# Performance work log

Hardware: AMD Instinct MI355X
Metric: run time of the kernel (lower is better)

## Reference

```python
import jax, jax.numpy as jnp
import numpy as np

B, T, D, H = 2, 2048, 2048, 16
HD = D // H


def setup_inputs() -> dict:
    key = jax.random.key(0)
    ks = jax.random.split(key, 6)
    s = 1.0 / np.sqrt(D)
    return {
        "x": jax.random.normal(ks[0], (B, T, D), dtype=jnp.float32),
        "Wq": jax.random.normal(ks[1], (D, D), dtype=jnp.float32) * s,
        "Wk": jax.random.normal(ks[2], (D, D), dtype=jnp.float32) * s,
        "Wv": jax.random.normal(ks[3], (D, D), dtype=jnp.float32) * s,
        "Wo": jax.random.normal(ks[4], (D, D), dtype=jnp.float32) * s,
        "bo": jnp.zeros((D,), dtype=jnp.float32),
    }


def reference(x, Wq, Wk, Wv, Wo, bo):
    b, t, d = x.shape
    # projections (torch Linear: x @ W.T)
    q = (x @ Wq.T).reshape(b, t, H, HD).transpose(0, 2, 1, 3)  # [B,H,T,HD]
    k = (x @ Wk.T).reshape(b, t, H, HD).transpose(0, 2, 1, 3)
    v = (x @ Wv.T).reshape(b, t, H, HD).transpose(0, 2, 1, 3)
    scores = jnp.einsum('bhid,bhjd->bhij', q, k) / np.sqrt(HD)  # [B,H,T,T]
    causal = jnp.tril(jnp.ones((t, t), dtype=bool))
    scores = jnp.where(causal[None, None], scores, -jnp.inf)
    attn = jax.nn.softmax(scores, axis=-1)
    out = jnp.einsum('bhij,bhjd->bhid', attn, v)  # [B,H,T,HD]
    out = out.transpose(0, 2, 1, 3).reshape(b, t, d)
    return out @ Wo.T + bo
```

## Files before the change

### kernel.cpp

```cpp
#include <hip/hip_runtime.h>
#include <hip/hip_bf16.h>

#define T_ 2048
#define D_ 2048
#define H_ 16
#define HD_ 128

typedef __hip_bfloat16 bf16;
using bf16x8 = __attribute__((ext_vector_type(8))) short;
using f32x4  = __attribute__((ext_vector_type(4))) float;

#define GLL16(g, l) __builtin_amdgcn_global_load_lds( \
    (const __attribute__((address_space(1))) void*)(g), \
    (__attribute__((address_space(3))) void*)(l), 16, 0, 0)

__device__ __forceinline__ f32x4 mfma16(bf16x8 a, bf16x8 b, f32x4 c) {
    return __builtin_amdgcn_mfma_f32_16x16x32_bf16(a, b, c, 0, 0, 0);
}

__global__ __launch_bounds__(256) void cast6(
    const float* __restrict__ s0, const float* __restrict__ s1,
    const float* __restrict__ s2, const float* __restrict__ s3,
    const float* __restrict__ s4, const float* __restrict__ s5,
    bf16* __restrict__ dst)
{
    int z = blockIdx.y;
    const float* s = (z == 0) ? s0 : (z == 1) ? s1 : (z == 2) ? s2
                   : (z == 3) ? s3 : (z == 4) ? s4 : s5;
    long i = ((long)blockIdx.x * 256 + threadIdx.x) * 8;
    float4 a = *(const float4*)(s + i);
    float4 b = *(const float4*)(s + i + 4);
    union { bf16 h[8]; int4 v; } u;
    u.h[0] = __float2bfloat16(a.x); u.h[1] = __float2bfloat16(a.y);
    u.h[2] = __float2bfloat16(a.z); u.h[3] = __float2bfloat16(a.w);
    u.h[4] = __float2bfloat16(b.x); u.h[5] = __float2bfloat16(b.y);
    u.h[6] = __float2bfloat16(b.z); u.h[7] = __float2bfloat16(b.w);
    *(int4*)(dst + (long)z * 4194304 + i) = u.v;
}


#define SA(t, h, b) do { \
    GLL16(Ab0 + (long)(h)*262144 + (t)*64,          &Asm[b][h][tid*8]); \
    GLL16(Ab0 + (long)(h)*262144 + 131072 + (t)*64, &Asm[b][h][4096 + tid*8]); \
} while (0)
#define SB(t, h, b) do { \
    GLL16(Bb0 + (long)(h)*262144 + (t)*64,          &Bsm[b][h][tid*8]); \
    GLL16(Bb0 + (long)(h)*262144 + 131072 + (t)*64, &Bsm[b][h][4096 + tid*8]); \
} while (0)

#define RA(mf, ks) (*(const bf16x8*)&Asm[buf][wr][((mf)*16 + l15)*64 + ((((ks)*32) + g8) ^ swF)])
#define RB(nf, ks) (*(const bf16x8*)&Bsm[buf][wc>>1][((wc&1)*64 + (nf)*16 + l15)*64 + ((((ks)*32) + g8) ^ swF)])

#define PH_SYNC() do { \
    __builtin_amdgcn_s_barrier(); \
    asm volatile("s_waitcnt lgkmcnt(0)" ::: "memory"); \
    __builtin_amdgcn_sched_barrier(0); \
} while (0)

__global__ __launch_bounds__(512) void gemm_qkv256(
    const bf16* __restrict__ xb, const bf16* __restrict__ Wall,
    bf16* __restrict__ QKV)
{
    __shared__ bf16 Asm[2][2][8192];
    __shared__ bf16 Bsm[2][2][8192];
    int tid = threadIdx.x, lane = tid & 63, wid = tid >> 6;
    int wr = wid >> 2, wc = wid & 3;
    int orig = blockIdx.x;
    int wg = (orig & 7) * 48 + (orig >> 3);
    int bm = wg / 24, bn = wg - bm * 24;

    int sr  = tid >> 3;
    int sc  = (((tid & 7) ^ (sr & 7)) * 8);
    const bf16* Ab0 = xb   + ((long)(bm * 256 + sr)) * 2048 + sc;
    const bf16* Bb0 = Wall + ((long)(bn * 256 + sr)) * 2048 + sc;

    int l15 = lane & 15, g8 = (lane >> 4) * 8;
    int swF = (l15 & 7) << 3;

    f32x4 acc[8][4];
    #pragma unroll
    for (int i = 0; i < 8; ++i)
        #pragma unroll
        for (int j = 0; j < 4; ++j) acc[i][j] = f32x4{0.f, 0.f, 0.f, 0.f};

    bf16x8 Ar[8][2];
    bf16x8 Br[4][2];

    SA(0, 0, 0); SA(0, 1, 0); SB(0, 0, 0); SB(0, 1, 0);
    SA(1, 0, 1); SA(1, 1, 1);
    asm volatile("s_waitcnt vmcnt(4)" ::: "memory");
    __builtin_amdgcn_s_barrier();

    const int NT = D_ / 64;
    for (int t = 0; t < NT; ++t) {
        int buf = t & 1, nbuf = buf ^ 1;
        #pragma unroll
        for (int mf = 0; mf < 4; ++mf) { Ar[mf][0] = RA(mf, 0); Ar[mf][1] = RA(mf, 1); }
        #pragma unroll
        for (int nf = 0; nf < 2; ++nf) { Br[nf][0] = RB(nf, 0); Br[nf][1] = RB(nf, 1); }
        if (t + 1 < NT) SB(t + 1, 0, nbuf);
        PH_SYNC();
        __builtin_amdgcn_s_setprio(1);
        #pragma unroll
        for (int mf = 0; mf < 4; ++mf)
            #pragma unroll
            for (int nf = 0; nf < 2; ++nf) {
                acc[mf][nf] = mfma16(Ar[mf][0], Br[nf][0], acc[mf][nf]);
                acc[mf][nf] = mfma16(Ar[mf][1], Br[nf][1], acc[mf][nf]);
            }
        __builtin_amdgcn_s_setprio(0);
        __builtin_amdgcn_s_barrier();
        #pragma unroll
        for (int mf = 4; mf < 8; ++mf) { Ar[mf][0] = RA(mf, 0); Ar[mf][1] = RA(mf, 1); }
        if (t + 1 < NT) SB(t + 1, 1, nbuf);
        PH_SYNC();
        __builtin_amdgcn_s_setprio(1);
        #pragma unroll
        for (int mf = 4; mf < 8; ++mf)
            #pragma unroll
            for (int nf = 0; nf < 2; ++nf) {
                acc[mf][nf] = mfma16(Ar[mf][0], Br[nf][0], acc[mf][nf]);
                acc[mf][nf] = mfma16(Ar[mf][1], Br[nf][1], acc[mf][nf]);
            }
        __builtin_amdgcn_s_setprio(0);
        __builtin_amdgcn_s_barrier();
        #pragma unroll
        for (int nf = 2; nf < 4; ++nf) { Br[nf][0] = RB(nf, 0); Br[nf][1] = RB(nf, 1); }
        if (t + 2 < NT) SA(t + 2, 0, buf);
        PH_SYNC();
        __builtin_amdgcn_s_setprio(1);
        #pragma unroll
        for (int mf = 0; mf < 4; ++mf)
            #pragma unroll
            for (int nf = 2; nf < 4; ++nf) {
                acc[mf][nf] = mfma16(Ar[mf][0], Br[nf][0], acc[mf][nf]);
                acc[mf][nf] = mfma16(Ar[mf][1], Br[nf][1], acc[mf][nf]);
            }
        __builtin_amdgcn_s_setprio(0);
        __builtin_amdgcn_s_barrier();
        if (t + 2 < NT) {
            SA(t + 2, 1, buf);
            asm volatile("s_waitcnt vmcnt(4)" ::: "memory");
        } else {
            asm volatile("s_waitcnt vmcnt(0)" ::: "memory");
        }
        __builtin_amdgcn_s_barrier();
        __builtin_amdgcn_s_setprio(1);
        #pragma unroll
        for (int mf = 4; mf < 8; ++mf)
            #pragma unroll
            for (int nf = 2; nf < 4; ++nf) {
                acc[mf][nf] = mfma16(Ar[mf][0], Br[nf][0], acc[mf][nf]);
                acc[mf][nf] = mfma16(Ar[mf][1], Br[nf][1], acc[mf][nf]);
            }
        __builtin_amdgcn_s_setprio(0);
        __builtin_amdgcn_s_barrier();
    }

    int mBase = bm * 256 + wr * 128;
    int nBase = bn * 256 + wc * 64;
    #pragma unroll
    for (int mf = 0; mf < 8; ++mf) {
        #pragma unroll
        for (int nf = 0; nf < 4; ++nf) {
            int n = nBase + nf * 16 + l15;
            int z = n >> 11, n2 = n & 2047;
            int h = n2 >> 7, hd = n2 & 127;
            #pragma unroll
            for (int r = 0; r < 4; ++r) {
                int m = mBase + mf * 16 + (lane >> 4) * 4 + r;
                int b = m >> 11, tt = m & 2047;
                QKV[(long)z * 8388608 + (((long)(b * H_ + h)) * T_ + tt) * HD_ + hd] =
                    __float2bfloat16(acc[mf][nf][r]);
            }
        }
    }
}


#define STAGE(t, b) do { \
    const bf16* Ag_ = Abase + (t)*32; \
    const bf16* Bg_ = Bbase + (t)*32; \
    GLL16(Ag_ + aoff0, As[b] + w*512); \
    GLL16(Ag_ + aoff1, As[b] + 2048 + w*512); \
    GLL16(Bg_ + aoff0, Bs[b] + w*512); \
    GLL16(Bg_ + aoff1, Bs[b] + 2048 + w*512); \
} while (0)

#define GEMM_MAINLOOP() \
    int tid = threadIdx.x, lane = tid & 63, w = tid >> 6; \
    int wm = w >> 1, wn = w & 1; \
    int srow = w*16 + (lane >> 2); \
    int scol = ((((lane & 3) - (srow >> 1)) & 3)) * 8; \
    long aoff0 = (long)srow * D_ + scol; \
    long aoff1 = aoff0 + 64L * D_; \
    f32x4 acc[4][4]; \
    _Pragma("unroll") \
    for (int i = 0; i < 4; ++i) \
        _Pragma("unroll") \
        for (int j = 0; j < 4; ++j) acc[i][j] = f32x4{0.f,0.f,0.f,0.f}; \
    STAGE(0, 0); STAGE(1, 1); STAGE(2, 2); \
    for (int kt = 0; kt < D_/32; ++kt) { \
        int rem = D_/32 - 1 - kt; \
        if (rem >= 2)      asm volatile("s_waitcnt vmcnt(8)" ::: "memory"); \
        else if (rem == 1) asm volatile("s_waitcnt vmcnt(4)" ::: "memory"); \
        else               asm volatile("s_waitcnt vmcnt(0)" ::: "memory"); \
        __builtin_amdgcn_s_barrier(); \
        asm volatile("" ::: "memory"); \
        int cb = kt & 3; \
        int g = lane >> 4; \
        bf16x8 af[4], bfr[4]; \
        _Pragma("unroll") \
        for (int mt = 0; mt < 4; ++mt) { \
            int r = wm*64 + mt*16 + (lane & 15); \
            af[mt] = *(const bf16x8*)&As[cb][r*32 + (((g + (r >> 1)) & 3) * 8)]; \
        } \
        _Pragma("unroll") \
        for (int nt = 0; nt < 4; ++nt) { \
            int r = wn*64 + nt*16 + (lane & 15); \
            bfr[nt] = *(const bf16x8*)&Bs[cb][r*32 + (((g + (r >> 1)) & 3) * 8)]; \
        } \
        if (kt + 3 < D_/32) { STAGE(kt + 3, (kt + 3) & 3); } \
        __builtin_amdgcn_s_setprio(1); \
        _Pragma("unroll") \
        for (int mt = 0; mt < 4; ++mt) \
            _Pragma("unroll") \
            for (int nt = 0; nt < 4; ++nt) \
                acc[mt][nt] = mfma16(af[mt], bfr[nt], acc[mt][nt]); \
        __builtin_amdgcn_s_setprio(0); \
    }

__global__ __launch_bounds__(256) void attn(
    const bf16* __restrict__ Qm, const bf16* __restrict__ Km, const bf16* __restrict__ Vm,
    bf16* __restrict__ Om)
{
    __shared__ bf16 Ks[64*136];
    __shared__ bf16 Vt[128*72];
    __shared__ bf16 Ps[128*72];
    int bm = 15 - (blockIdx.x >> 5);
    int bh = blockIdx.x & 31;
    int tid = threadIdx.x, lane = tid & 63, w = tid >> 6;
    const float c1 = 0.12754012780914427f;
    const float c2 = 23.083120654223414f;
    const bf16* Qb = Qm + (long)bh*T_*HD_;
    const bf16* Kb = Km + (long)bh*T_*HD_;
    const bf16* Vb = Vm + (long)bh*T_*HD_;
    int m0 = bm*128 + w*32;

    bf16x8 qf[2][4];
    #pragma unroll
    for (int mt = 0; mt < 2; ++mt)
        #pragma unroll
        for (int ks = 0; ks < 4; ++ks)
            qf[mt][ks] = *(const bf16x8*)(Qb + (long)(m0 + mt*16 + (lane & 15))*HD_ + ks*32 + (lane >> 4)*8);

    bf16x8 onesB;
    {
        short v1 = ((lane & 15) == 0) ? (short)0x3F80 : (short)0;
        #pragma unroll
        for (int jj = 0; jj < 8; ++jj) onesB[jj] = v1;
    }

    f32x4 oacc[2][8];
    f32x4 lacc[2];
    #pragma unroll
    for (int mt = 0; mt < 2; ++mt) {
        lacc[mt] = f32x4{0.f,0.f,0.f,0.f};
        #pragma unroll
        for (int dt = 0; dt < 8; ++dt) oacc[mt][dt] = f32x4{0.f,0.f,0.f,0.f};
    }

    int krow = (tid >> 4);
    int kcg  = tid & 15;
    int njt = 2*bm + 2;

    bf16x8 kreg[4], vreg[4];
    #pragma unroll
    for (int i = 0; i < 4; ++i) {
        kreg[i] = *(const bf16x8*)(Kb + (long)(i*16 + krow)*HD_ + kcg*8);
        vreg[i] = *(const bf16x8*)(Vb + (long)lane*HD_ + (w + i*4)*8);
    }

    for (int j = 0; j < njt; ++j) {
        int j0 = j*64;
        __syncthreads();
        #pragma unroll
        for (int i = 0; i < 4; ++i)
            *(bf16x8*)&Ks[(i*16 + krow)*136 + kcg*8] = kreg[i];
        #pragma unroll
        for (int i = 0; i < 4; ++i) {
            int dg = w + i*4;
            union { bf16 h[8]; bf16x8 v; } u;
            u.v = vreg[i];
            #pragma unroll
            for (int jj = 0; jj < 8; ++jj)
                Vt[(dg*8 + jj)*72 + lane] = u.h[jj];
        }
        __syncthreads();

        if (j + 1 < njt) {
            int jn0 = j0 + 64;
            #pragma unroll
            for (int i = 0; i < 4; ++i) {
                kreg[i] = *(const bf16x8*)(Kb + (long)(jn0 + i*16 + krow)*HD_ + kcg*8);
                vreg[i] = *(const bf16x8*)(Vb + (long)(jn0 + lane)*HD_ + (w + i*4)*8);
            }
        }

        bool anyv  = (j0 <= m0 + 31);
        if (anyv) {
            bool bmask = (j0 + 63 > m0);
            f32x4 s[2][4];
            #pragma unroll
            for (int mt = 0; mt < 2; ++mt)
                #pragma unroll
                for (int nt = 0; nt < 4; ++nt) s[mt][nt] = f32x4{0.f,0.f,0.f,0.f};
            #pragma unroll
            for (int ks = 0; ks < 4; ++ks) {
                bf16x8 kf[4];
                #pragma unroll
                for (int nt = 0; nt < 4; ++nt)
                    kf[nt] = *(const bf16x8*)&Ks[(nt*16 + (lane & 15))*136 + ks*32 + (lane >> 4)*8];
                #pragma unroll
                for (int mt = 0; mt < 2; ++mt)
                    #pragma unroll
                    for (int nt = 0; nt < 4; ++nt)
                        s[mt][nt] = mfma16(qf[mt][ks], kf[nt], s[mt][nt]);
            }
            #pragma unroll
            for (int mt = 0; mt < 2; ++mt) {
                #pragma unroll
                for (int nt = 0; nt < 4; ++nt) {
                    int n = j0 + nt*16 + (lane & 15);
                    #pragma unroll
                    for (int r = 0; r < 4; ++r) {
                        float x = s[mt][nt][r] * c1 - c2;
                        if (bmask) {
                            int mg = m0 + mt*16 + (lane >> 4)*4 + r;
                            x = (n <= mg) ? x : -1e30f;
                        }
                        float p = exp2f(x);
                        int prow = w*32 + mt*16 + (lane >> 4)*4 + r;
                        Ps[prow*72 + nt*16 + (lane & 15)] = __float2bfloat16(p);
                    }
                }
            }
            #pragma unroll
            for (int kn = 0; kn < 2; ++kn) {
                bf16x8 pf[2], vf[8];
                #pragma unroll
                for (int mt = 0; mt < 2; ++mt)
                    pf[mt] = *(const bf16x8*)&Ps[(w*32 + mt*16 + (lane & 15))*72 + kn*32 + (lane >> 4)*8];
                #pragma unroll
                for (int dt = 0; dt < 8; ++dt)
                    vf[dt] = *(const bf16x8*)&Vt[(dt*16 + (lane & 15))*72 + kn*32 + (lane >> 4)*8];
                #pragma unroll
                for (int mt = 0; mt < 2; ++mt)
                    lacc[mt] = mfma16(pf[mt], onesB, lacc[mt]);
                #pragma unroll
                for (int mt = 0; mt < 2; ++mt)
                    #pragma unroll
                    for (int dt = 0; dt < 8; ++dt)
                        oacc[mt][dt] = mfma16(pf[mt], vf[dt], oacc[mt][dt]);
            }
        }
    }
    int b = bh >> 4, h = bh & 15;
    #pragma unroll
    for (int mt = 0; mt < 2; ++mt) {
        #pragma unroll
        for (int r = 0; r < 4; ++r) {
            float l = __shfl(lacc[mt][r], lane & 48, 64);
            float inv = 1.f / l;
            int t = m0 + mt*16 + (lane >> 4)*4 + r;
            #pragma unroll
            for (int dt = 0; dt < 8; ++dt) {
                int d = dt*16 + (lane & 15);
                Om[((long)(b*T_ + t))*D_ + h*HD_ + d] = __float2bfloat16(oacc[mt][dt][r] * inv);
            }
        }
    }
}

__global__ __launch_bounds__(256) void gemm_out(
    const bf16* __restrict__ Ab, const bf16* __restrict__ Wob,
    const float* __restrict__ bo, float* __restrict__ out)
{
    __shared__ bf16 As[4][128*32];
    __shared__ bf16 Bs[4][128*32];
    int bn = blockIdx.x, bm = blockIdx.y;
    const bf16* Abase = Ab  + (long)bm * 128 * D_;
    const bf16* Bbase = Wob + (long)bn * 128 * D_;

    GEMM_MAINLOOP();

    int mlo = bm*128 + wm*64;
    int nlo = bn*128 + wn*64;
    #pragma unroll
    for (int mt = 0; mt < 4; ++mt) {
        #pragma unroll
        for (int nt = 0; nt < 4; ++nt) {
            int n = nlo + nt*16 + (lane & 15);
            float bias = bo[n];
            #pragma unroll
            for (int r = 0; r < 4; ++r) {
                int m = mlo + mt*16 + (lane >> 4)*4 + r;
                out[(long)m*D_ + n] = acc[mt][nt][r] + bias;
            }
        }
    }
}

extern "C" void kernel_launch(void* const* d_in, const int* in_sizes, int n_in,
                              void* d_out, int out_size, void* d_ws, size_t ws_size,
                              hipStream_t stream) {
    const float* x  = (const float*)d_in[0];
    const float* Wq = (const float*)d_in[1];
    const float* Wk = (const float*)d_in[2];
    const float* Wv = (const float*)d_in[3];
    const float* Wo = (const float*)d_in[4];
    const float* bo = (const float*)d_in[5];
    float* out = (float*)d_out;

    bf16* ws  = (bf16*)d_ws;
    bf16* xb  = ws;
    bf16* wqb = ws + 8388608L;
    bf16* wob = ws + 20971520L;
    bf16* Qb  = ws + 25165824L;
    bf16* Kb  = ws + 33554432L;
    bf16* Vb  = ws + 41943040L;
    bf16* Ob  = xb;

    cast6<<<dim3(2048, 6), 256, 0, stream>>>(x, x + 4194304L, Wq, Wk, Wv, Wo, ws);
    gemm_qkv256<<<dim3(384), 512, 0, stream>>>(xb, wqb, Qb);
    attn<<<512, 256, 0, stream>>>(Qb, Kb, Vb, Ob);
    gemm_out<<<dim3(16, 32), 256, 0, stream>>>(Ob, wob, bo, out);
}
```

Measured before the change: 405.0 us.

## Retile QKV projection GEMM to 128x384 blocks with 512-block grid

Replaces the 256x256 QKV projection tile with a 128x384 tile, launching 512 workgroups instead of 384. This should balance waves across the 256 CUs, since 384 blocks leave a partial second wave. The per-wave fragment changes to 4x6 MFMA tiles, the LDS staging and prefetch schedule is reworked for one A and six B chunks per k-step, and the grid swizzle is updated. The trade-off is lower arithmetic intensity per block and more B traffic.

```diff
diff --git a/kernel.cpp b/kernel.cpp
--- a/kernel.cpp
+++ b/kernel.cpp
@@ -39,17 +39,11 @@
 }
 
 
-#define SA(t, h, b) do { \
-    GLL16(Ab0 + (long)(h)*262144 + (t)*64,          &Asm[b][h][tid*8]); \
-    GLL16(Ab0 + (long)(h)*262144 + 131072 + (t)*64, &Asm[b][h][4096 + tid*8]); \
-} while (0)
-#define SB(t, h, b) do { \
-    GLL16(Bb0 + (long)(h)*262144 + (t)*64,          &Bsm[b][h][tid*8]); \
-    GLL16(Bb0 + (long)(h)*262144 + 131072 + (t)*64, &Bsm[b][h][4096 + tid*8]); \
-} while (0)
-
-#define RA(mf, ks) (*(const bf16x8*)&Asm[buf][wr][((mf)*16 + l15)*64 + ((((ks)*32) + g8) ^ swF)])
-#define RB(nf, ks) (*(const bf16x8*)&Bsm[buf][wc>>1][((wc&1)*64 + (nf)*16 + l15)*64 + ((((ks)*32) + g8) ^ swF)])
+#define SA2(t, c, b) GLL16(Ab0 + (long)(c)*131072 + (t)*64, &Asm[b][c][wu])
+#define SB2(t, c, b) GLL16(Bb0 + (long)(c)*131072 + (t)*64, &Bsm[b][c][wu])
+
+#define RA2(mf, ks) (*(const bf16x8*)&Asm[buf][wr][((mf)*16 + l15)*64 + ((((ks)*32) + g8) ^ swF)])
+#define RB2(nf, ks) (*(const bf16x8*)&Bsm[buf][(wc*96 + (nf)*16) >> 6][(((wc*96 + (nf)*16) & 63) + l15)*64 + ((((ks)*32) + g8) ^ swF)])
 
 #define PH_SYNC() do { \
     __builtin_amdgcn_s_barrier(); \
@@ -57,112 +51,111 @@
     __builtin_amdgcn_sched_barrier(0); \
 } while (0)
 
-__global__ __launch_bounds__(512) void gemm_qkv256(
+__global__ __launch_bounds__(512) void gemm_qkv384(
     const bf16* __restrict__ xb, const bf16* __restrict__ Wall,
     bf16* __restrict__ QKV)
 {
-    __shared__ bf16 Asm[2][2][8192];
-    __shared__ bf16 Bsm[2][2][8192];
+    __shared__ bf16 Asm[2][2][4096];
+    __shared__ bf16 Bsm[2][6][4096];
     int tid = threadIdx.x, lane = tid & 63, wid = tid >> 6;
     int wr = wid >> 2, wc = wid & 3;
+    int wu = wid * 512;
     int orig = blockIdx.x;
-    int wg = (orig & 7) * 48 + (orig >> 3);
-    int bm = wg / 24, bn = wg - bm * 24;
+    int wg = (orig & 7) * 64 + (orig >> 3);
+    int bm = wg >> 4, bn = wg & 15;
 
     int sr  = tid >> 3;
     int sc  = (((tid & 7) ^ (sr & 7)) * 8);
-    const bf16* Ab0 = xb   + ((long)(bm * 256 + sr)) * 2048 + sc;
-    const bf16* Bb0 = Wall + ((long)(bn * 256 + sr)) * 2048 + sc;
+    const bf16* Ab0 = xb   + ((long)(bm * 128 + sr)) * 2048 + sc;
+    const bf16* Bb0 = Wall + ((long)(bn * 384 + sr)) * 2048 + sc;
 
     int l15 = lane & 15, g8 = (lane >> 4) * 8;
     int swF = (l15 & 7) << 3;
 
-    f32x4 acc[8][4];
-    #pragma unroll
-    for (int i = 0; i < 8; ++i)
-        #pragma unroll
-        for (int j = 0; j < 4; ++j) acc[i][j] = f32x4{0.f, 0.f, 0.f, 0.f};
-
-    bf16x8 Ar[8][2];
-    bf16x8 Br[4][2];
-
-    SA(0, 0, 0); SA(0, 1, 0); SB(0, 0, 0); SB(0, 1, 0);
-    SA(1, 0, 1); SA(1, 1, 1);
-    asm volatile("s_waitcnt vmcnt(4)" ::: "memory");
+    f32x4 acc[4][6];
+    #pragma unroll
+    for (int i = 0; i < 4; ++i)
+        #pragma unroll
+        for (int j = 0; j < 6; ++j) acc[i][j] = f32x4{0.f, 0.f, 0.f, 0.f};
+
+    bf16x8 Ar0[4], Ar1[4];
+    bf16x8 Br[3];
+
+    SA2(0, 0, 0); SA2(0, 1, 0);
+    SB2(0, 0, 0); SB2(0, 1, 0); SB2(0, 2, 0);
+    SB2(0, 3, 0); SB2(0, 4, 0); SB2(0, 5, 0);
+    SA2(1, 0, 1); SA2(1, 1, 1);
+    asm volatile("s_waitcnt vmcnt(2)" ::: "memory");
     __builtin_amdgcn_s_barrier();
 
     const int NT = D_ / 64;
     for (int t = 0; t < NT; ++t) {
         int buf = t & 1, nbuf = buf ^ 1;
         #pragma unroll
-        for (int mf = 0; mf < 4; ++mf) { Ar[mf][0] = RA(mf, 0); Ar[mf][1] = RA(mf, 1); }
-        #pragma unroll
-        for (int nf = 0; nf < 2; ++nf) { Br[nf][0] = RB(nf, 0); Br[nf][1] = RB(nf, 1); }
-        if (t + 1 < NT) SB(t + 1, 0, nbuf);
+        for (int mf = 0; mf < 4; ++mf) Ar0[mf] = RA2(mf, 0);
+        #pragma unroll
+        for (int nf = 0; nf < 3; ++nf) Br[nf] = RB2(nf, 0);
+        if (t + 1 < NT) { SB2(t + 1, 0, nbuf); SB2(t + 1, 1, nbuf); }
         PH_SYNC();
         __builtin_amdgcn_s_setprio(1);
         #pragma unroll
         for (int mf = 0; mf < 4; ++mf)
             #pragma unroll
-            for (int nf = 0; nf < 2; ++nf) {
-                acc[mf][nf] = mfma16(Ar[mf][0], Br[nf][0], acc[mf][nf]);
-                acc[mf][nf] = mfma16(Ar[mf][1], Br[nf][1], acc[mf][nf]);
-            }
+            for (int nf = 0; nf < 3; ++nf)
+                acc[mf][nf] = mfma16(Ar0[mf], Br[nf], acc[mf][nf]);
         __builtin_amdgcn_s_setprio(0);
         __builtin_amdgcn_s_barrier();
         #pragma unroll
-        for (int mf = 4; mf < 8; ++mf) { Ar[mf][0] = RA(mf, 0); Ar[mf][1] = RA(mf, 1); }
-        if (t + 1 < NT) SB(t + 1, 1, nbuf);
+        for (int nf = 0; nf < 3; ++nf) Br[nf] = RB2(nf + 3, 0);
+        if (t + 1 < NT) { SB2(t + 1, 2, nbuf); SB2(t + 1, 3, nbuf); }
         PH_SYNC();
         __builtin_amdgcn_s_setprio(1);
         #pragma unroll
-        for (int mf = 4; mf < 8; ++mf)
-            #pragma unroll
-            for (int nf = 0; nf < 2; ++nf) {
-                acc[mf][nf] = mfma16(Ar[mf][0], Br[nf][0], acc[mf][nf]);
-                acc[mf][nf] = mfma16(Ar[mf][1], Br[nf][1], acc[mf][nf]);
-            }
+        for (int mf = 0; mf < 4; ++mf)
+            #pragma unroll
+            for (int nf = 0; nf < 3; ++nf)
+                acc[mf][nf + 3] = mfma16(Ar0[mf], Br[nf], acc[mf][nf + 3]);
         __builtin_amdgcn_s_setprio(0);
         __builtin_amdgcn_s_barrier();
         #pragma unroll
-        for (int nf = 2; nf < 4; ++nf) { Br[nf][0] = RB(nf, 0); Br[nf][1] = RB(nf, 1); }
-        if (t + 2 < NT) SA(t + 2, 0, buf);
+        for (int mf = 0; mf < 4; ++mf) Ar1[mf] = RA2(mf, 1);
+        #pragma unroll
+        for (int nf = 0; nf < 3; ++nf) Br[nf] = RB2(nf, 1);
+        if (t + 1 < NT) { SB2(t + 1, 4, nbuf); SB2(t + 1, 5, nbuf); }
         PH_SYNC();
         __builtin_amdgcn_s_setprio(1);
         #pragma unroll
         for (int mf = 0; mf < 4; ++mf)
             #pragma unroll
-            for (int nf = 2; nf < 4; ++nf) {
-                acc[mf][nf] = mfma16(Ar[mf][0], Br[nf][0], acc[mf][nf]);
-                acc[mf][nf] = mfma16(Ar[mf][1], Br[nf][1], acc[mf][nf]);
-            }
+            for (int nf = 0; nf < 3; ++nf)
+                acc[mf][nf] = mfma16(Ar1[mf], Br[nf], acc[mf][nf]);
         __builtin_amdgcn_s_setprio(0);
         __builtin_amdgcn_s_barrier();
+        #pragma unroll
+        for (int nf = 0; nf < 3; ++nf) Br[nf] = RB2(nf + 3, 1);
         if (t + 2 < NT) {
-            SA(t + 2, 1, buf);
-            asm volatile("s_waitcnt vmcnt(4)" ::: "memory");
+            SA2(t + 2, 0, buf); SA2(t + 2, 1, buf);
+            asm volatile("s_waitcnt vmcnt(2)" ::: "memory");
         } else {
             asm volatile("s_waitcnt vmcnt(0)" ::: "memory");
         }
-        __builtin_amdgcn_s_barrier();
+        PH_SYNC();
         __builtin_amdgcn_s_setprio(1);
         #pragma unroll
-        for (int mf = 4; mf < 8; ++mf)
-            #pragma unroll
-            for (int nf = 2; nf < 4; ++nf) {
-                acc[mf][nf] = mfma16(Ar[mf][0], Br[nf][0], acc[mf][nf]);
-                acc[mf][nf] = mfma16(Ar[mf][1], Br[nf][1], acc[mf][nf]);
-            }
+        for (int mf = 0; mf < 4; ++mf)
+            #pragma unroll
+            for (int nf = 0; nf < 3; ++nf)
+                acc[mf][nf + 3] = mfma16(Ar1[mf], Br[nf], acc[mf][nf + 3]);
         __builtin_amdgcn_s_setprio(0);
         __builtin_amdgcn_s_barrier();
     }
 
-    int mBase = bm * 256 + wr * 128;
-    int nBase = bn * 256 + wc * 64;
-    #pragma unroll
-    for (int mf = 0; mf < 8; ++mf) {
-        #pragma unroll
-        for (int nf = 0; nf < 4; ++nf) {
+    int mBase = bm * 128 + wr * 64;
+    int nBase = bn * 384 + wc * 96;
+    #pragma unroll
+    for (int mf = 0; mf < 4; ++mf) {
+        #pragma unroll
+        for (int nf = 0; nf < 6; ++nf) {
             int n = nBase + nf * 16 + l15;
             int z = n >> 11, n2 = n & 2047;
             int h = n2 >> 7, hd = n2 & 127;
@@ -432,7 +425,7 @@
     bf16* Ob  = xb;
 
     cast6<<<dim3(2048, 6), 256, 0, stream>>>(x, x + 4194304L, Wq, Wk, Wv, Wo, ws);
-    gemm_qkv256<<<dim3(384), 512, 0, stream>>>(xb, wqb, Qb);
+    gemm_qkv384<<<dim3(512), 512, 0, stream>>>(xb, wqb, Qb);
     attn<<<512, 256, 0, stream>>>(Qb, Kb, Vb, Ob);
     gemm_out<<<dim3(16, 32), 256, 0, stream>>>(Ob, wob, bo, out);
 }
```

Measured after the change: 399.8 us. No clear change (-1.3%).
